# Kernel tuning notes

Hardware: AMD Instinct MI355X
Metric: run time of the kernel (lower is better)

Reference implementation:

```python
import jax, jax.numpy as jnp
import numpy as np

B, T, D_MODEL = 2, 192, 512
N_HEADS, D_HEAD = 8, 64
IGNORE = -1000000.0


def setup_inputs() -> dict:
    key = jax.random.key(0)
    ks = jax.random.split(key, 5)
    s = 0.02
    return {
        "x": jax.random.normal(ks[0], (B, T, D_MODEL), dtype=jnp.float32),
        "Wkkq": jax.random.normal(ks[1], (D_MODEL, 3 * N_HEADS * D_HEAD), dtype=jnp.float32) * s,
        "bkkq": jnp.zeros((3 * N_HEADS * D_HEAD,), jnp.float32),
        "Wv1": jax.random.normal(ks[2], (D_MODEL, N_HEADS * D_HEAD), dtype=jnp.float32) * s,
        "bv1": jnp.zeros((N_HEADS * D_HEAD,), jnp.float32),
        "Wv2": jax.random.normal(ks[3], (D_MODEL, N_HEADS * D_HEAD), dtype=jnp.float32) * s,
        "bv2": jnp.zeros((N_HEADS * D_HEAD,), jnp.float32),
        "Wout": jax.random.normal(ks[4], (N_HEADS * D_HEAD, D_MODEL), dtype=jnp.float32) * s,
        "bout": jnp.zeros((D_MODEL,), jnp.float32),
    }


def reference(x, Wkkq, bkkq, Wv1, bv1, Wv2, bv2, Wout, bout):
    b, ts, _ = x.shape
    kkq = x @ Wkkq + bkkq                          # [b, t, 3*n*h]
    k1, k2, q = jnp.split(kkq, 3, axis=-1)
    rs = lambda a: a.reshape(b, ts, N_HEADS, D_HEAD)  # b p n h
    k1, k2, q = rs(k1), rs(k2), rs(q)

    v1 = (x @ Wv1 + bv1).reshape(b, ts, N_HEADS, D_HEAD)
    v2 = (x @ Wv2 + bv2).reshape(b, ts, N_HEADS, D_HEAD)

    # third-order scores: [b, n, s, t, q]
    score_qk = jnp.einsum('btnh,bqnh->bntq', k2, q)   # [b, n, t, q]
    score_kk = jnp.einsum('bsnh,btnh->bnst', k1, k2)  # [b, n, s, t]
    score = score_qk[:, :, None, :, :] + score_kk[..., None]  # [b,n,s,t,q]

    idx = jnp.arange(ts)
    # causal mask: (t > q) | (s > q)  over axes (s, t, q)
    mask = (idx[:, None, None] > idx[None, None, :]) | (idx[None, :, None] > idx[None, None, :])
    score = jnp.where(mask[None, None], IGNORE, score)

    # b n s t q -> b n q (s t), scale by d_head, softmax over flattened (s,t)
    score = jnp.transpose(score, (0, 1, 4, 2, 3)).reshape(b, N_HEADS, ts, ts * ts)
    attn = jax.nn.softmax(score / D_HEAD, axis=-1)

    # v[b, p, t, n, h] = silu(v1)[b,p,n,h] * v2[b,t,n,h]
    v = jax.nn.silu(v1)[:, :, None] * v2[:, None]     # [b, p, t, n, h]
    v = jnp.transpose(v, (0, 3, 4, 1, 2)).reshape(b, N_HEADS, D_HEAD, ts * ts)

    z = jnp.einsum('bnql,bnhl->bqnh', attn, v)        # [b, q, n, h]
    out = z.reshape(b, ts, N_HEADS * D_HEAD) @ Wout + bout
    return out
```

## Files before the change

kernel.cpp:

```cpp
#include <hip/hip_runtime.h>
#include <hip/hip_bf16.h>


constexpr int Tn = 192;
constexpr int DM = 512;
constexpr int NH = 8;
constexpr int HD = 64;
constexpr int TT = Tn * Tn;
constexpr int NCc = 6;
constexpr int CSc = 32;

typedef __bf16 bf16_t;
typedef bf16_t bf16x8 __attribute__((ext_vector_type(8)));
typedef float  f32x4  __attribute__((ext_vector_type(4)));

struct bf16pair { bf16_t h, l; };
__device__ __forceinline__ bf16pair split_bf16(float v) {
    bf16pair r;
    r.h = (bf16_t)v;
    r.l = (bf16_t)(v - (float)r.h);
    return r;
}

__global__ __launch_bounds__(256) void k_projm(
    const float* __restrict__ x,
    const float* __restrict__ Wkkq, const float* __restrict__ Wv1,
    const float* __restrict__ Wv2,
    const float* __restrict__ bkkq, const float* __restrict__ bv1,
    const float* __restrict__ bv2,
    float* __restrict__ k1, float* __restrict__ k2, float* __restrict__ qv,
    float* __restrict__ sv1, float* __restrict__ v2o)
{
    const int bx = blockIdx.x, by = blockIdx.y;
    const int tid = threadIdx.x;
    const int w = tid >> 6, lane = tid & 63;
    const int wm = w & 1, wn = w >> 1;
    const int lr = lane & 15, lk = (lane >> 4) * 8;

    const float* Wp; int ldw, cloc;
    if (bx < 48)      { Wp = Wkkq; ldw = 1536; cloc = bx * 32; }
    else if (bx < 64) { Wp = Wv1;  ldw = 512;  cloc = bx * 32 - 1536; }
    else              { Wp = Wv2;  ldw = 512;  cloc = bx * 32 - 2048; }

    const int arow = by * 32 + wm * 16 + lr;
    const int bcol = cloc + wn * 16 + lr;
    const float* xrow = x + arow * DM;

    f32x4 acc = {0.f,0.f,0.f,0.f};
    bf16x8 A_ah, A_al, A_bh, A_bl;
    bf16x8 B_ah, B_al, B_bh, B_bl;

#define PLD(P_, KS) do { const int ko_ = (KS) * 32 + lk;                                  \
    const float4 u0 = *reinterpret_cast<const float4*>(&xrow[ko_]);                       \
    const float4 u1 = *reinterpret_cast<const float4*>(&xrow[ko_ + 4]);                   \
    const float* wp_ = Wp + ko_ * ldw + bcol;                                             \
    const float w0_ = wp_[0],       w1_ = wp_[ldw],     w2_ = wp_[2 * ldw];               \
    const float w3_ = wp_[3 * ldw], w4_ = wp_[4 * ldw], w5_ = wp_[5 * ldw];               \
    const float w6_ = wp_[6 * ldw], w7_ = wp_[7 * ldw];                                   \
    bf16pair t0_ = split_bf16(u0.x), t1_ = split_bf16(u0.y);                              \
    bf16pair t2_ = split_bf16(u0.z), t3_ = split_bf16(u0.w);                              \
    bf16pair t4_ = split_bf16(u1.x), t5_ = split_bf16(u1.y);                              \
    bf16pair t6_ = split_bf16(u1.z), t7_ = split_bf16(u1.w);                              \
    P_##ah[0] = t0_.h; P_##al[0] = t0_.l; P_##ah[1] = t1_.h; P_##al[1] = t1_.l;           \
    P_##ah[2] = t2_.h; P_##al[2] = t2_.l; P_##ah[3] = t3_.h; P_##al[3] = t3_.l;           \
    P_##ah[4] = t4_.h; P_##al[4] = t4_.l; P_##ah[5] = t5_.h; P_##al[5] = t5_.l;           \
    P_##ah[6] = t6_.h; P_##al[6] = t6_.l; P_##ah[7] = t7_.h; P_##al[7] = t7_.l;           \
    bf16pair s0_ = split_bf16(w0_), s1_ = split_bf16(w1_);                                \
    bf16pair s2_ = split_bf16(w2_), s3_ = split_bf16(w3_);                                \
    bf16pair s4_ = split_bf16(w4_), s5_ = split_bf16(w5_);                                \
    bf16pair s6_ = split_bf16(w6_), s7_ = split_bf16(w7_);                                \
    P_##bh[0] = s0_.h; P_##bl[0] = s0_.l; P_##bh[1] = s1_.h; P_##bl[1] = s1_.l;           \
    P_##bh[2] = s2_.h; P_##bl[2] = s2_.l; P_##bh[3] = s3_.h; P_##bl[3] = s3_.l;           \
    P_##bh[4] = s4_.h; P_##bl[4] = s4_.l; P_##bh[5] = s5_.h; P_##bl[5] = s5_.l;           \
    P_##bh[6] = s6_.h; P_##bl[6] = s6_.l; P_##bh[7] = s7_.h; P_##bl[7] = s7_.l; } while (0)
#define PMM(P_) do {                                                                    \
    acc = __builtin_amdgcn_mfma_f32_16x16x32_bf16(P_##ah, P_##bh, acc, 0, 0, 0);        \
    acc = __builtin_amdgcn_mfma_f32_16x16x32_bf16(P_##ah, P_##bl, acc, 0, 0, 0);        \
    acc = __builtin_amdgcn_mfma_f32_16x16x32_bf16(P_##al, P_##bh, acc, 0, 0, 0); } while (0)
#define PSTEP(P_, KN) do { PMM(P_); if ((KN) < 16) PLD(P_, KN); } while (0)

    PLD(A_, 0); PLD(B_, 1);
    PSTEP(A_, 2);  PSTEP(B_, 3);  PSTEP(A_, 4);  PSTEP(B_, 5);
    PSTEP(A_, 6);  PSTEP(B_, 7);  PSTEP(A_, 8);  PSTEP(B_, 9);
    PSTEP(A_, 10); PSTEP(B_, 11); PSTEP(A_, 12); PSTEP(B_, 13);
    PSTEP(A_, 14); PSTEP(B_, 15); PSTEP(A_, 16); PSTEP(B_, 17);
#undef PLD
#undef PMM
#undef PSTEP

    const int gcol = bx * 32 + wn * 16 + lr;
#pragma unroll
    for (int r = 0; r < 4; ++r) {
        const int row = by * 32 + wm * 16 + (lane >> 4) * 4 + r;
        const int b = row / Tn, t = row % Tn;
        const float a = acc[r];
        if (gcol < 1536) {
            const float val = a + bkkq[gcol];
            const int third = gcol >> 9, nh = gcol & 511, n = nh >> 6, hh = nh & 63;
            float* dst = (third == 0) ? k1 : (third == 1) ? k2 : qv;
            dst[((b * NH + n) * Tn + t) * HD + hh] = val;
        } else if (gcol < 2048) {
            const int c = gcol - 1536;
            float val = a + bv1[c];
            val = val / (1.f + __expf(-val));
            sv1[((b * NH + (c >> 6)) * Tn + t) * HD + (c & 63)] = val;
        } else {
            const int c = gcol - 2048;
            v2o[((b * NH + (c >> 6)) * Tn + t) * HD + (c & 63)] = a + bv2[c];
        }
    }
}

__global__ __launch_bounds__(256) void k_scoresP(
    const float* __restrict__ k1, const float* __restrict__ k2,
    const float* __restrict__ qv, const float* __restrict__ sv1,
    float* __restrict__ Ekk, float* __restrict__ Eqk,
    float* __restrict__ P, float* __restrict__ gP)
{
    const int bn = blockIdx.y;
    int bx = blockIdx.x;
    const int mat = (bx >= 36) ? 1 : 0;
    if (mat) bx -= 36;
    const int st = bx / 6, tt = bx % 6;
    const float* A  = ((mat == 0) ? k1 : qv) + bn * Tn * HD;
    const float* Bm = k2 + bn * Tn * HD;
    float* E = ((mat == 0) ? Ekk : Eqk) + bn * TT;

    __shared__ float As[32][65], Bs[32][65], Vs[32][65];
    __shared__ float Es[32][33];
    const int tid = threadIdx.x;
    for (int i = tid; i < 32 * 64; i += 256) {
        const int r = i >> 6, h = i & 63;
        As[r][h] = A[(st * 32 + r) * HD + h];
        Bs[r][h] = Bm[(tt * 32 + r) * HD + h];
        if (mat == 0) Vs[r][h] = sv1[bn * Tn * HD + (st * 32 + r) * HD + h];
    }
    __syncthreads();

    const int tx = tid & 15, ty = tid >> 4;
    const int r0 = ty * 2, c0 = tx * 2;
    float a00 = 0.f, a01 = 0.f, a10 = 0.f, a11 = 0.f;
#pragma unroll
    for (int h = 0; h < 64; ++h) {
        const float ar0 = As[r0][h], ar1 = As[r0 + 1][h];
        const float bc0 = Bs[c0][h], bc1 = Bs[c0 + 1][h];
        a00 = fmaf(ar0, bc0, a00); a01 = fmaf(ar0, bc1, a01);
        a10 = fmaf(ar1, bc0, a10); a11 = fmaf(ar1, bc1, a11);
    }
    constexpr float sc = 1.f / 64.f;
    const float e00 = __expf(a00 * sc), e01 = __expf(a01 * sc);
    const float e10 = __expf(a10 * sc), e11 = __expf(a11 * sc);
    const int gr = st * 32 + r0, gc = tt * 32 + c0;
    E[(gr)     * Tn + gc]     = e00;
    E[(gr)     * Tn + gc + 1] = e01;
    E[(gr + 1) * Tn + gc]     = e10;
    E[(gr + 1) * Tn + gc + 1] = e11;

    if (mat == 0) {
        Es[r0][c0] = e00; Es[r0][c0 + 1] = e01;
        Es[r0 + 1][c0] = e10; Es[r0 + 1][c0 + 1] = e11;
        __syncthreads();

        const int h   = tid >> 2;
        const int tp0 = (tid & 3) * 8;
        float p[8] = {0.f,0.f,0.f,0.f,0.f,0.f,0.f,0.f};
        for (int s = 0; s < 32; ++s) {
            const float a = Vs[s][h];
#pragma unroll
            for (int j = 0; j < 8; ++j) p[j] = fmaf(Es[s][tp0 + j], a, p[j]);
        }
        float* pd = P + ((bn * NCc + st) * HD + h) * Tn + tt * 32 + tp0;
        *reinterpret_cast<float4*>(&pd[0]) = make_float4(p[0], p[1], p[2], p[3]);
        *reinterpret_cast<float4*>(&pd[4]) = make_float4(p[4], p[5], p[6], p[7]);

        if (tid < 32) {
            float s = 0.f;
#pragma unroll
            for (int ss = 0; ss < 32; ++ss) s += Es[ss][tid];
            gP[(bn * NCc + st) * Tn + tt * 32 + tid] = s;
        }
    }
}

__global__ __launch_bounds__(256) void k_attn2(
    const float* __restrict__ Ekk, const float* __restrict__ Eqk,
    const float* __restrict__ sv1, const float* __restrict__ v2,
    const float* __restrict__ P,   const float* __restrict__ gP,
    float* __restrict__ z)
{
    const int hq = blockIdx.x;
    const int qt = blockIdx.y;
    const int bn = blockIdx.z;
    const int b = bn >> 3, n = bn & 7;
    const int tid = threadIdx.x;
    const int tg  = tid & 15;
    const int hh  = tid >> 4;
    const int h   = hq * 16 + hh;
    const int t0  = tg * 12;
    const int q0  = qt * 12;
    const int cb  = q0 >> 5;

    const float* ekk = Ekk + bn * TT;
    const float* eqk = Eqk + bn * TT;
    const float* s1  = sv1 + bn * Tn * HD;
    const float* vv  = v2  + bn * Tn * HD;

    float G[12], g[12];
#pragma unroll
    for (int j = 0; j < 12; ++j) { G[j] = 0.f; g[j] = 0.f; }

    for (int c = 0; c < cb; ++c) {
        const float* pb = P  + ((bn * NCc + c) * HD + h) * Tn + t0;
        const float* gb = gP + (bn * NCc + c) * Tn + t0;
#pragma unroll
        for (int jj = 0; jj < 3; ++jj) {
            const float4 pv = *reinterpret_cast<const float4*>(&pb[4 * jj]);
            G[4*jj+0] += pv.x; G[4*jj+1] += pv.y; G[4*jj+2] += pv.z; G[4*jj+3] += pv.w;
            const float4 gv = *reinterpret_cast<const float4*>(&gb[4 * jj]);
            g[4*jj+0] += gv.x; g[4*jj+1] += gv.y; g[4*jj+2] += gv.z; g[4*jj+3] += gv.w;
        }
    }

    float vvr[12];
#pragma unroll
    for (int j = 0; j < 12; ++j) vvr[j] = vv[(t0 + j) * HD + h];

    for (int s = CSc * cb; s < q0; ++s) {
        const float a = s1[s * HD + h];
        const float* ek = ekk + s * Tn + t0;
#pragma unroll
        for (int jj = 0; jj < 3; ++jj) {
            const float4 ev = *reinterpret_cast<const float4*>(&ek[4 * jj]);
            G[4*jj+0] = fmaf(ev.x, a, G[4*jj+0]); g[4*jj+0] += ev.x;
            G[4*jj+1] = fmaf(ev.y, a, G[4*jj+1]); g[4*jj+1] += ev.y;
            G[4*jj+2] = fmaf(ev.z, a, G[4*jj+2]); g[4*jj+2] += ev.z;
            G[4*jj+3] = fmaf(ev.w, a, G[4*jj+3]); g[4*jj+3] += ev.w;
        }
    }

    for (int q = q0; q < q0 + 12; ++q) {
        {
            const float a = s1[q * HD + h];
            const float* ek = ekk + q * Tn + t0;
#pragma unroll
            for (int jj = 0; jj < 3; ++jj) {
                const float4 ev = *reinterpret_cast<const float4*>(&ek[4 * jj]);
                G[4*jj+0] = fmaf(ev.x, a, G[4*jj+0]); g[4*jj+0] += ev.x;
                G[4*jj+1] = fmaf(ev.y, a, G[4*jj+1]); g[4*jj+1] += ev.y;
                G[4*jj+2] = fmaf(ev.z, a, G[4*jj+2]); g[4*jj+2] += ev.z;
                G[4*jj+3] = fmaf(ev.w, a, G[4*jj+3]); g[4*jj+3] += ev.w;
            }
        }
        const float* eq = eqk + q * Tn + t0;
        float zp = 0.f, Zp = 0.f;
#pragma unroll
        for (int jj = 0; jj < 3; ++jj) {
            const float4 ev = *reinterpret_cast<const float4*>(&eq[4 * jj]);
            const float e0 = (t0 + 4*jj + 0 <= q) ? ev.x : 0.f;
            const float e1 = (t0 + 4*jj + 1 <= q) ? ev.y : 0.f;
            const float e2 = (t0 + 4*jj + 2 <= q) ? ev.z : 0.f;
            const float e3 = (t0 + 4*jj + 3 <= q) ? ev.w : 0.f;
            zp = fmaf(e0 * vvr[4*jj+0], G[4*jj+0], zp); Zp = fmaf(e0, g[4*jj+0], Zp);
            zp = fmaf(e1 * vvr[4*jj+1], G[4*jj+1], zp); Zp = fmaf(e1, g[4*jj+1], Zp);
            zp = fmaf(e2 * vvr[4*jj+2], G[4*jj+2], zp); Zp = fmaf(e2, g[4*jj+2], Zp);
            zp = fmaf(e3 * vvr[4*jj+3], G[4*jj+3], zp); Zp = fmaf(e3, g[4*jj+3], Zp);
        }
        zp += __shfl_xor(zp, 1); zp += __shfl_xor(zp, 2);
        zp += __shfl_xor(zp, 4); zp += __shfl_xor(zp, 8);
        Zp += __shfl_xor(Zp, 1); Zp += __shfl_xor(Zp, 2);
        Zp += __shfl_xor(Zp, 4); Zp += __shfl_xor(Zp, 8);
        if (tg == 0) z[((b * Tn + q) * NH + n) * HD + h] = zp / Zp;
    }
}

__global__ __launch_bounds__(256) void k_outm(
    const float* __restrict__ z, const float* __restrict__ Wout,
    const float* __restrict__ bout, float* __restrict__ out)
{
    const int bx = blockIdx.x, by = blockIdx.y;
    const int tid = threadIdx.x;
    const int w = tid >> 6, lane = tid & 63;
    const int lr = lane & 15, lk = (lane >> 4) * 8;
    const int arow = by * 16 + lr;
    const int bcol = bx * 64 + w * 16 + lr;
    const float* zrow = z + arow * DM;

    f32x4 acc = {0.f,0.f,0.f,0.f};
    bf16x8 A_ah, A_al, A_bh, A_bl;
    bf16x8 B_ah, B_al, B_bh, B_bl;

#define OLD(P_, KS) do { const int ko_ = (KS) * 32 + lk;                                  \
    const float4 u0 = *reinterpret_cast<const float4*>(&zrow[ko_]);                       \
    const float4 u1 = *reinterpret_cast<const float4*>(&zrow[ko_ + 4]);                   \
    const float* wp_ = Wout + ko_ * DM + bcol;                                            \
    const float w0_ = wp_[0],      w1_ = wp_[DM],     w2_ = wp_[2 * DM];                  \
    const float w3_ = wp_[3 * DM], w4_ = wp_[4 * DM], w5_ = wp_[5 * DM];                  \
    const float w6_ = wp_[6 * DM], w7_ = wp_[7 * DM];                                     \
    bf16pair t0_ = split_bf16(u0.x), t1_ = split_bf16(u0.y);                              \
    bf16pair t2_ = split_bf16(u0.z), t3_ = split_bf16(u0.w);                              \
    bf16pair t4_ = split_bf16(u1.x), t5_ = split_bf16(u1.y);                              \
    bf16pair t6_ = split_bf16(u1.z), t7_ = split_bf16(u1.w);                              \
    P_##ah[0] = t0_.h; P_##al[0] = t0_.l; P_##ah[1] = t1_.h; P_##al[1] = t1_.l;           \
    P_##ah[2] = t2_.h; P_##al[2] = t2_.l; P_##ah[3] = t3_.h; P_##al[3] = t3_.l;           \
    P_##ah[4] = t4_.h; P_##al[4] = t4_.l; P_##ah[5] = t5_.h; P_##al[5] = t5_.l;           \
    P_##ah[6] = t6_.h; P_##al[6] = t6_.l; P_##ah[7] = t7_.h; P_##al[7] = t7_.l;           \
    bf16pair s0_ = split_bf16(w0_), s1_ = split_bf16(w1_);                                \
    bf16pair s2_ = split_bf16(w2_), s3_ = split_bf16(w3_);                                \
    bf16pair s4_ = split_bf16(w4_), s5_ = split_bf16(w5_);                                \
    bf16pair s6_ = split_bf16(w6_), s7_ = split_bf16(w7_);                                \
    P_##bh[0] = s0_.h; P_##bl[0] = s0_.l; P_##bh[1] = s1_.h; P_##bl[1] = s1_.l;           \
    P_##bh[2] = s2_.h; P_##bl[2] = s2_.l; P_##bh[3] = s3_.h; P_##bl[3] = s3_.l;           \
    P_##bh[4] = s4_.h; P_##bl[4] = s4_.l; P_##bh[5] = s5_.h; P_##bl[5] = s5_.l;           \
    P_##bh[6] = s6_.h; P_##bl[6] = s6_.l; P_##bh[7] = s7_.h; P_##bl[7] = s7_.l; } while (0)
#define OMM(P_) do {                                                                   \
    acc = __builtin_amdgcn_mfma_f32_16x16x32_bf16(P_##ah, P_##bh, acc, 0, 0, 0);       \
    acc = __builtin_amdgcn_mfma_f32_16x16x32_bf16(P_##ah, P_##bl, acc, 0, 0, 0);       \
    acc = __builtin_amdgcn_mfma_f32_16x16x32_bf16(P_##al, P_##bh, acc, 0, 0, 0); } while (0)
#define OSTEP(P_, KN) do { OMM(P_); if ((KN) < 16) OLD(P_, KN); } while (0)

    OLD(A_, 0); OLD(B_, 1);
    OSTEP(A_, 2);  OSTEP(B_, 3);  OSTEP(A_, 4);  OSTEP(B_, 5);
    OSTEP(A_, 6);  OSTEP(B_, 7);  OSTEP(A_, 8);  OSTEP(B_, 9);
    OSTEP(A_, 10); OSTEP(B_, 11); OSTEP(A_, 12); OSTEP(B_, 13);
    OSTEP(A_, 14); OSTEP(B_, 15); OSTEP(A_, 16); OSTEP(B_, 17);
#undef OLD
#undef OMM
#undef OSTEP

#pragma unroll
    for (int r = 0; r < 4; ++r) {
        const int row = by * 16 + (lane >> 4) * 4 + r;
        out[row * DM + bcol] = acc[r] + bout[bcol];
    }
}

extern "C" void kernel_launch(void* const* d_in, const int* in_sizes, int n_in,
                              void* d_out, int out_size, void* d_ws, size_t ws_size,
                              hipStream_t stream) {
    const float* x    = (const float*)d_in[0];
    const float* Wkkq = (const float*)d_in[1];
    const float* bkkq = (const float*)d_in[2];
    const float* Wv1  = (const float*)d_in[3];
    const float* bv1  = (const float*)d_in[4];
    const float* Wv2  = (const float*)d_in[5];
    const float* bv2  = (const float*)d_in[6];
    const float* Wout = (const float*)d_in[7];
    const float* bout = (const float*)d_in[8];
    float* out = (float*)d_out;

    float* ws  = (float*)d_ws;
    float* k1  = ws;
    float* k2  = k1  + 196608;
    float* qv  = k2  + 196608;
    float* sv1 = qv  + 196608;
    float* v2  = sv1 + 196608;
    float* z   = v2  + 196608;
    float* Ekk = z   + 196608;
    float* Eqk = Ekk + 589824;
    float* P   = Eqk + 589824;
    float* gP  = P   + 1179648;

    k_projm  <<<dim3(80, 12),    256, 0, stream>>>(x, Wkkq, Wv1, Wv2,
                                                   bkkq, bv1, bv2,
                                                   k1, k2, qv, sv1, v2);
    k_scoresP<<<dim3(72, 16),    256, 0, stream>>>(k1, k2, qv, sv1, Ekk, Eqk, P, gP);
    k_attn2  <<<dim3(4, 16, 16), 256, 0, stream>>>(Ekk, Eqk, sv1, v2, P, gP, z);
    k_outm   <<<dim3(8, 24),     256, 0, stream>>>(z, Wout, bout, out);
}
```

Measured before the change: 83.98 us.

## Fuse four kernels into one persistent cooperative kernel with grid syncs

```diff
diff --git a/kernel.cpp b/kernel.cpp
--- a/kernel.cpp
+++ b/kernel.cpp
@@ -1,5 +1,8 @@
 #include <hip/hip_runtime.h>
 #include <hip/hip_bf16.h>
+#include <hip/hip_cooperative_groups.h>
+
+namespace cg = cooperative_groups;
 
 
 constexpr int Tn = 192;
@@ -22,33 +25,35 @@
     return r;
 }
 
-__global__ __launch_bounds__(256) void k_projm(
+__device__ __forceinline__ void phase1(
     const float* __restrict__ x,
     const float* __restrict__ Wkkq, const float* __restrict__ Wv1,
     const float* __restrict__ Wv2,
     const float* __restrict__ bkkq, const float* __restrict__ bv1,
     const float* __restrict__ bv2,
     float* __restrict__ k1, float* __restrict__ k2, float* __restrict__ qv,
-    float* __restrict__ sv1, float* __restrict__ v2o)
-{
-    const int bx = blockIdx.x, by = blockIdx.y;
-    const int tid = threadIdx.x;
+    float* __restrict__ sv1, float* __restrict__ v2o,
+    int bid0, int nblk, int tid)
+{
     const int w = tid >> 6, lane = tid & 63;
     const int wm = w & 1, wn = w >> 1;
     const int lr = lane & 15, lk = (lane >> 4) * 8;
 
-    const float* Wp; int ldw, cloc;
-    if (bx < 48)      { Wp = Wkkq; ldw = 1536; cloc = bx * 32; }
-    else if (bx < 64) { Wp = Wv1;  ldw = 512;  cloc = bx * 32 - 1536; }
-    else              { Wp = Wv2;  ldw = 512;  cloc = bx * 32 - 2048; }
-
-    const int arow = by * 32 + wm * 16 + lr;
-    const int bcol = cloc + wn * 16 + lr;
-    const float* xrow = x + arow * DM;
-
-    f32x4 acc = {0.f,0.f,0.f,0.f};
-    bf16x8 A_ah, A_al, A_bh, A_bl;
-    bf16x8 B_ah, B_al, B_bh, B_bl;
+    for (int wi = bid0; wi < 960; wi += nblk) {
+        const int bx = wi % 80, by = wi / 80;
+
+        const float* Wp; int ldw, cloc;
+        if (bx < 48)      { Wp = Wkkq; ldw = 1536; cloc = bx * 32; }
+        else if (bx < 64) { Wp = Wv1;  ldw = 512;  cloc = bx * 32 - 1536; }
+        else              { Wp = Wv2;  ldw = 512;  cloc = bx * 32 - 2048; }
+
+        const int arow = by * 32 + wm * 16 + lr;
+        const int bcol = cloc + wn * 16 + lr;
+        const float* xrow = x + arow * DM;
+
+        f32x4 acc = {0.f,0.f,0.f,0.f};
+        bf16x8 A_ah, A_al, A_bh, A_bl;
+        bf16x8 B_ah, B_al, B_bh, B_bl;
 
 #define PLD(P_, KS) do { const int ko_ = (KS) * 32 + lk;                                  \
     const float4 u0 = *reinterpret_cast<const float4*>(&xrow[ko_]);                       \
@@ -79,169 +84,160 @@
     acc = __builtin_amdgcn_mfma_f32_16x16x32_bf16(P_##al, P_##bh, acc, 0, 0, 0); } while (0)
 #define PSTEP(P_, KN) do { PMM(P_); if ((KN) < 16) PLD(P_, KN); } while (0)
 
-    PLD(A_, 0); PLD(B_, 1);
-    PSTEP(A_, 2);  PSTEP(B_, 3);  PSTEP(A_, 4);  PSTEP(B_, 5);
-    PSTEP(A_, 6);  PSTEP(B_, 7);  PSTEP(A_, 8);  PSTEP(B_, 9);
-    PSTEP(A_, 10); PSTEP(B_, 11); PSTEP(A_, 12); PSTEP(B_, 13);
-    PSTEP(A_, 14); PSTEP(B_, 15); PSTEP(A_, 16); PSTEP(B_, 17);
+        PLD(A_, 0); PLD(B_, 1);
+        PSTEP(A_, 2);  PSTEP(B_, 3);  PSTEP(A_, 4);  PSTEP(B_, 5);
+        PSTEP(A_, 6);  PSTEP(B_, 7);  PSTEP(A_, 8);  PSTEP(B_, 9);
+        PSTEP(A_, 10); PSTEP(B_, 11); PSTEP(A_, 12); PSTEP(B_, 13);
+        PSTEP(A_, 14); PSTEP(B_, 15); PSTEP(A_, 16); PSTEP(B_, 17);
 #undef PLD
 #undef PMM
 #undef PSTEP
 
-    const int gcol = bx * 32 + wn * 16 + lr;
-#pragma unroll
-    for (int r = 0; r < 4; ++r) {
-        const int row = by * 32 + wm * 16 + (lane >> 4) * 4 + r;
-        const int b = row / Tn, t = row % Tn;
-        const float a = acc[r];
-        if (gcol < 1536) {
-            const float val = a + bkkq[gcol];
-            const int third = gcol >> 9, nh = gcol & 511, n = nh >> 6, hh = nh & 63;
-            float* dst = (third == 0) ? k1 : (third == 1) ? k2 : qv;
-            dst[((b * NH + n) * Tn + t) * HD + hh] = val;
-        } else if (gcol < 2048) {
-            const int c = gcol - 1536;
-            float val = a + bv1[c];
-            val = val / (1.f + __expf(-val));
-            sv1[((b * NH + (c >> 6)) * Tn + t) * HD + (c & 63)] = val;
-        } else {
-            const int c = gcol - 2048;
-            v2o[((b * NH + (c >> 6)) * Tn + t) * HD + (c & 63)] = a + bv2[c];
-        }
-    }
-}
-
-__global__ __launch_bounds__(256) void k_scoresP(
+        const int gcol = bx * 32 + wn * 16 + lr;
+#pragma unroll
+        for (int r = 0; r < 4; ++r) {
+            const int row = by * 32 + wm * 16 + (lane >> 4) * 4 + r;
+            const int b = row / Tn, t = row % Tn;
+            const float a = acc[r];
+            if (gcol < 1536) {
+                const float val = a + bkkq[gcol];
+                const int third = gcol >> 9, nh = gcol & 511, n = nh >> 6, hh = nh & 63;
+                float* dst = (third == 0) ? k1 : (third == 1) ? k2 : qv;
+                dst[((b * NH + n) * Tn + t) * HD + hh] = val;
+            } else if (gcol < 2048) {
+                const int c = gcol - 1536;
+                float val = a + bv1[c];
+                val = val / (1.f + __expf(-val));
+                sv1[((b * NH + (c >> 6)) * Tn + t) * HD + (c & 63)] = val;
+            } else {
+                const int c = gcol - 2048;
+                v2o[((b * NH + (c >> 6)) * Tn + t) * HD + (c & 63)] = a + bv2[c];
+            }
+        }
+    }
+}
+
+__device__ __forceinline__ void phase2(
     const float* __restrict__ k1, const float* __restrict__ k2,
     const float* __restrict__ qv, const float* __restrict__ sv1,
     float* __restrict__ Ekk, float* __restrict__ Eqk,
-    float* __restrict__ P, float* __restrict__ gP)
-{
-    const int bn = blockIdx.y;
-    int bx = blockIdx.x;
-    const int mat = (bx >= 36) ? 1 : 0;
-    if (mat) bx -= 36;
-    const int st = bx / 6, tt = bx % 6;
-    const float* A  = ((mat == 0) ? k1 : qv) + bn * Tn * HD;
-    const float* Bm = k2 + bn * Tn * HD;
-    float* E = ((mat == 0) ? Ekk : Eqk) + bn * TT;
-
+    float* __restrict__ P, float* __restrict__ gP,
+    int bid0, int nblk, int tid)
+{
     __shared__ float As[32][65], Bs[32][65], Vs[32][65];
     __shared__ float Es[32][33];
-    const int tid = threadIdx.x;
-    for (int i = tid; i < 32 * 64; i += 256) {
-        const int r = i >> 6, h = i & 63;
-        As[r][h] = A[(st * 32 + r) * HD + h];
-        Bs[r][h] = Bm[(tt * 32 + r) * HD + h];
-        if (mat == 0) Vs[r][h] = sv1[bn * Tn * HD + (st * 32 + r) * HD + h];
-    }
-    __syncthreads();
-
-    const int tx = tid & 15, ty = tid >> 4;
-    const int r0 = ty * 2, c0 = tx * 2;
-    float a00 = 0.f, a01 = 0.f, a10 = 0.f, a11 = 0.f;
-#pragma unroll
-    for (int h = 0; h < 64; ++h) {
-        const float ar0 = As[r0][h], ar1 = As[r0 + 1][h];
-        const float bc0 = Bs[c0][h], bc1 = Bs[c0 + 1][h];
-        a00 = fmaf(ar0, bc0, a00); a01 = fmaf(ar0, bc1, a01);
-        a10 = fmaf(ar1, bc0, a10); a11 = fmaf(ar1, bc1, a11);
-    }
-    constexpr float sc = 1.f / 64.f;
-    const float e00 = __expf(a00 * sc), e01 = __expf(a01 * sc);
-    const float e10 = __expf(a10 * sc), e11 = __expf(a11 * sc);
-    const int gr = st * 32 + r0, gc = tt * 32 + c0;
-    E[(gr)     * Tn + gc]     = e00;
-    E[(gr)     * Tn + gc + 1] = e01;
-    E[(gr + 1) * Tn + gc]     = e10;
-    E[(gr + 1) * Tn + gc + 1] = e11;
-
-    if (mat == 0) {
-        Es[r0][c0] = e00; Es[r0][c0 + 1] = e01;
-        Es[r0 + 1][c0] = e10; Es[r0 + 1][c0 + 1] = e11;
+
+    for (int wi = bid0; wi < 1152; wi += nblk) {
+        const int bn = wi / 72;
+        int bx = wi % 72;
+        const int mat = (bx >= 36) ? 1 : 0;
+        if (mat) bx -= 36;
+        const int st = bx / 6, tt = bx % 6;
+        const float* A  = ((mat == 0) ? k1 : qv) + bn * Tn * HD;
+        const float* Bm = k2 + bn * Tn * HD;
+        float* E = ((mat == 0) ? Ekk : Eqk) + bn * TT;
+
+        for (int i = tid; i < 32 * 64; i += 256) {
+            const int r = i >> 6, h = i & 63;
+            As[r][h] = A[(st * 32 + r) * HD + h];
+            Bs[r][h] = Bm[(tt * 32 + r) * HD + h];
+            if (mat == 0) Vs[r][h] = sv1[bn * Tn * HD + (st * 32 + r) * HD + h];
+        }
         __syncthreads();
 
-        const int h   = tid >> 2;
-        const int tp0 = (tid & 3) * 8;
-        float p[8] = {0.f,0.f,0.f,0.f,0.f,0.f,0.f,0.f};
-        for (int s = 0; s < 32; ++s) {
-            const float a = Vs[s][h];
-#pragma unroll
-            for (int j = 0; j < 8; ++j) p[j] = fmaf(Es[s][tp0 + j], a, p[j]);
-        }
-        float* pd = P + ((bn * NCc + st) * HD + h) * Tn + tt * 32 + tp0;
-        *reinterpret_cast<float4*>(&pd[0]) = make_float4(p[0], p[1], p[2], p[3]);
-        *reinterpret_cast<float4*>(&pd[4]) = make_float4(p[4], p[5], p[6], p[7]);
-
-        if (tid < 32) {
-            float s = 0.f;
-#pragma unroll
-            for (int ss = 0; ss < 32; ++ss) s += Es[ss][tid];
-            gP[(bn * NCc + st) * Tn + tt * 32 + tid] = s;
-        }
-    }
-}
-
-__global__ __launch_bounds__(256) void k_attn2(
+        const int tx = tid & 15, ty = tid >> 4;
+        const int r0 = ty * 2, c0 = tx * 2;
+        float a00 = 0.f, a01 = 0.f, a10 = 0.f, a11 = 0.f;
+#pragma unroll
+        for (int h = 0; h < 64; ++h) {
+            const float ar0 = As[r0][h], ar1 = As[r0 + 1][h];
+            const float bc0 = Bs[c0][h], bc1 = Bs[c0 + 1][h];
+            a00 = fmaf(ar0, bc0, a00); a01 = fmaf(ar0, bc1, a01);
+            a10 = fmaf(ar1, bc0, a10); a11 = fmaf(ar1, bc1, a11);
+        }
+        constexpr float sc = 1.f / 64.f;
+        const float e00 = __expf(a00 * sc), e01 = __expf(a01 * sc);
+        const float e10 = __expf(a10 * sc), e11 = __expf(a11 * sc);
+        const int gr = st * 32 + r0, gc = tt * 32 + c0;
+        E[(gr)     * Tn + gc]     = e00;
+        E[(gr)     * Tn + gc + 1] = e01;
+        E[(gr + 1) * Tn + gc]     = e10;
+        E[(gr + 1) * Tn + gc + 1] = e11;
+
+        if (mat == 0) {
+            Es[r0][c0] = e00; Es[r0][c0 + 1] = e01;
+            Es[r0 + 1][c0] = e10; Es[r0 + 1][c0 + 1] = e11;
+            __syncthreads();
+
+            const int h   = tid >> 2;
+            const int tp0 = (tid & 3) * 8;
+            float p[8] = {0.f,0.f,0.f,0.f,0.f,0.f,0.f,0.f};
+            for (int s = 0; s < 32; ++s) {
+                const float a = Vs[s][h];
+#pragma unroll
+                for (int j = 0; j < 8; ++j) p[j] = fmaf(Es[s][tp0 + j], a, p[j]);
+            }
+            float* pd = P + ((bn * NCc + st) * HD + h) * Tn + tt * 32 + tp0;
+            *reinterpret_cast<float4*>(&pd[0]) = make_float4(p[0], p[1], p[2], p[3]);
+            *reinterpret_cast<float4*>(&pd[4]) = make_float4(p[4], p[5], p[6], p[7]);
+
+            if (tid < 32) {
+                float s = 0.f;
+#pragma unroll
+                for (int ss = 0; ss < 32; ++ss) s += Es[ss][tid];
+                gP[(bn * NCc + st) * Tn + tt * 32 + tid] = s;
+            }
+        }
+        __syncthreads();
+    }
+}
+
+__device__ __forceinline__ void phase3(
     const float* __restrict__ Ekk, const float* __restrict__ Eqk,
-    const float* __restrict__ sv1, const float* __restrict__ v2,
+    const float* __restrict__ sv1, const float* __restrict__ v2o,
     const float* __restrict__ P,   const float* __restrict__ gP,
-    float* __restrict__ z)
-{
-    const int hq = blockIdx.x;
-    const int qt = blockIdx.y;
-    const int bn = blockIdx.z;
-    const int b = bn >> 3, n = bn & 7;
-    const int tid = threadIdx.x;
-    const int tg  = tid & 15;
-    const int hh  = tid >> 4;
-    const int h   = hq * 16 + hh;
-    const int t0  = tg * 12;
-    const int q0  = qt * 12;
-    const int cb  = q0 >> 5;
-
-    const float* ekk = Ekk + bn * TT;
-    const float* eqk = Eqk + bn * TT;
-    const float* s1  = sv1 + bn * Tn * HD;
-    const float* vv  = v2  + bn * Tn * HD;
-
-    float G[12], g[12];
-#pragma unroll
-    for (int j = 0; j < 12; ++j) { G[j] = 0.f; g[j] = 0.f; }
-
-    for (int c = 0; c < cb; ++c) {
-        const float* pb = P  + ((bn * NCc + c) * HD + h) * Tn + t0;
-        const float* gb = gP + (bn * NCc + c) * Tn + t0;
-#pragma unroll
-        for (int jj = 0; jj < 3; ++jj) {
-            const float4 pv = *reinterpret_cast<const float4*>(&pb[4 * jj]);
-            G[4*jj+0] += pv.x; G[4*jj+1] += pv.y; G[4*jj+2] += pv.z; G[4*jj+3] += pv.w;
-            const float4 gv = *reinterpret_cast<const float4*>(&gb[4 * jj]);
-            g[4*jj+0] += gv.x; g[4*jj+1] += gv.y; g[4*jj+2] += gv.z; g[4*jj+3] += gv.w;
-        }
-    }
-
-    float vvr[12];
-#pragma unroll
-    for (int j = 0; j < 12; ++j) vvr[j] = vv[(t0 + j) * HD + h];
-
-    for (int s = CSc * cb; s < q0; ++s) {
-        const float a = s1[s * HD + h];
-        const float* ek = ekk + s * Tn + t0;
-#pragma unroll
-        for (int jj = 0; jj < 3; ++jj) {
-            const float4 ev = *reinterpret_cast<const float4*>(&ek[4 * jj]);
-            G[4*jj+0] = fmaf(ev.x, a, G[4*jj+0]); g[4*jj+0] += ev.x;
-            G[4*jj+1] = fmaf(ev.y, a, G[4*jj+1]); g[4*jj+1] += ev.y;
-            G[4*jj+2] = fmaf(ev.z, a, G[4*jj+2]); g[4*jj+2] += ev.z;
-            G[4*jj+3] = fmaf(ev.w, a, G[4*jj+3]); g[4*jj+3] += ev.w;
-        }
-    }
-
-    for (int q = q0; q < q0 + 12; ++q) {
-        {
-            const float a = s1[q * HD + h];
-            const float* ek = ekk + q * Tn + t0;
+    float* __restrict__ z,
+    int bid0, int nblk, int tid)
+{
+    const int tg = tid & 15, hh = tid >> 4;
+    for (int wi = bid0; wi < 1024; wi += nblk) {
+        const int hq = wi & 3;
+        const int qt = (wi >> 2) & 15;
+        const int bn = wi >> 6;
+        const int b = bn >> 3, n = bn & 7;
+        const int h  = hq * 16 + hh;
+        const int t0 = tg * 12;
+        const int q0 = qt * 12;
+        const int cb = q0 >> 5;
+
+        const float* ekk = Ekk + bn * TT;
+        const float* eqk = Eqk + bn * TT;
+        const float* s1  = sv1 + bn * Tn * HD;
+        const float* vv  = v2o + bn * Tn * HD;
+
+        float G[12], g[12];
+#pragma unroll
+        for (int j = 0; j < 12; ++j) { G[j] = 0.f; g[j] = 0.f; }
+
+        for (int c = 0; c < cb; ++c) {
+            const float* pb = P  + ((bn * NCc + c) * HD + h) * Tn + t0;
+            const float* gb = gP + (bn * NCc + c) * Tn + t0;
+#pragma unroll
+            for (int jj = 0; jj < 3; ++jj) {
+                const float4 pv = *reinterpret_cast<const float4*>(&pb[4 * jj]);
+                G[4*jj+0] += pv.x; G[4*jj+1] += pv.y; G[4*jj+2] += pv.z; G[4*jj+3] += pv.w;
+                const float4 gv = *reinterpret_cast<const float4*>(&gb[4 * jj]);
+                g[4*jj+0] += gv.x; g[4*jj+1] += gv.y; g[4*jj+2] += gv.z; g[4*jj+3] += gv.w;
+            }
+        }
+
+        float vvr[12];
+#pragma unroll
+        for (int j = 0; j < 12; ++j) vvr[j] = vv[(t0 + j) * HD + h];
+
+        for (int s = CSc * cb; s < q0; ++s) {
+            const float a = s1[s * HD + h];
+            const float* ek = ekk + s * Tn + t0;
 #pragma unroll
             for (int jj = 0; jj < 3; ++jj) {
                 const float4 ev = *reinterpret_cast<const float4*>(&ek[4 * jj]);
@@ -251,43 +247,59 @@
                 G[4*jj+3] = fmaf(ev.w, a, G[4*jj+3]); g[4*jj+3] += ev.w;
             }
         }
-        const float* eq = eqk + q * Tn + t0;
-        float zp = 0.f, Zp = 0.f;
-#pragma unroll
-        for (int jj = 0; jj < 3; ++jj) {
-            const float4 ev = *reinterpret_cast<const float4*>(&eq[4 * jj]);
-            const float e0 = (t0 + 4*jj + 0 <= q) ? ev.x : 0.f;
-            const float e1 = (t0 + 4*jj + 1 <= q) ? ev.y : 0.f;
-            const float e2 = (t0 + 4*jj + 2 <= q) ? ev.z : 0.f;
-            const float e3 = (t0 + 4*jj + 3 <= q) ? ev.w : 0.f;
-            zp = fmaf(e0 * vvr[4*jj+0], G[4*jj+0], zp); Zp = fmaf(e0, g[4*jj+0], Zp);
-            zp = fmaf(e1 * vvr[4*jj+1], G[4*jj+1], zp); Zp = fmaf(e1, g[4*jj+1], Zp);
-            zp = fmaf(e2 * vvr[4*jj+2], G[4*jj+2], zp); Zp = fmaf(e2, g[4*jj+2], Zp);
-            zp = fmaf(e3 * vvr[4*jj+3], G[4*jj+3], zp); Zp = fmaf(e3, g[4*jj+3], Zp);
-        }
-        zp += __shfl_xor(zp, 1); zp += __shfl_xor(zp, 2);
-        zp += __shfl_xor(zp, 4); zp += __shfl_xor(zp, 8);
-        Zp += __shfl_xor(Zp, 1); Zp += __shfl_xor(Zp, 2);
-        Zp += __shfl_xor(Zp, 4); Zp += __shfl_xor(Zp, 8);
-        if (tg == 0) z[((b * Tn + q) * NH + n) * HD + h] = zp / Zp;
-    }
-}
-
-__global__ __launch_bounds__(256) void k_outm(
+
+        for (int q = q0; q < q0 + 12; ++q) {
+            {
+                const float a = s1[q * HD + h];
+                const float* ek = ekk + q * Tn + t0;
+#pragma unroll
+                for (int jj = 0; jj < 3; ++jj) {
+                    const float4 ev = *reinterpret_cast<const float4*>(&ek[4 * jj]);
+                    G[4*jj+0] = fmaf(ev.x, a, G[4*jj+0]); g[4*jj+0] += ev.x;
+                    G[4*jj+1] = fmaf(ev.y, a, G[4*jj+1]); g[4*jj+1] += ev.y;
+                    G[4*jj+2] = fmaf(ev.z, a, G[4*jj+2]); g[4*jj+2] += ev.z;
+                    G[4*jj+3] = fmaf(ev.w, a, G[4*jj+3]); g[4*jj+3] += ev.w;
+                }
+            }
+            const float* eq = eqk + q * Tn + t0;
+            float zp = 0.f, Zp = 0.f;
+#pragma unroll
+            for (int jj = 0; jj < 3; ++jj) {
+                const float4 ev = *reinterpret_cast<const float4*>(&eq[4 * jj]);
+                const float e0 = (t0 + 4*jj + 0 <= q) ? ev.x : 0.f;
+                const float e1 = (t0 + 4*jj + 1 <= q) ? ev.y : 0.f;
+                const float e2 = (t0 + 4*jj + 2 <= q) ? ev.z : 0.f;
+                const float e3 = (t0 + 4*jj + 3 <= q) ? ev.w : 0.f;
+                zp = fmaf(e0 * vvr[4*jj+0], G[4*jj+0], zp); Zp = fmaf(e0, g[4*jj+0], Zp);
+                zp = fmaf(e1 * vvr[4*jj+1], G[4*jj+1], zp); Zp = fmaf(e1, g[4*jj+1], Zp);
+                zp = fmaf(e2 * vvr[4*jj+2], G[4*jj+2], zp); Zp = fmaf(e2, g[4*jj+2], Zp);
+                zp = fmaf(e3 * vvr[4*jj+3], G[4*jj+3], zp); Zp = fmaf(e3, g[4*jj+3], Zp);
+            }
+            zp += __shfl_xor(zp, 1); zp += __shfl_xor(zp, 2);
+            zp += __shfl_xor(zp, 4); zp += __shfl_xor(zp, 8);
+            Zp += __shfl_xor(Zp, 1); Zp += __shfl_xor(Zp, 2);
+            Zp += __shfl_xor(Zp, 4); Zp += __shfl_xor(Zp, 8);
+            if (tg == 0) z[((b * Tn + q) * NH + n) * HD + h] = zp / Zp;
+        }
+    }
+}
+
+__device__ __forceinline__ void phase4(
     const float* __restrict__ z, const float* __restrict__ Wout,
-    const float* __restrict__ bout, float* __restrict__ out)
-{
-    const int bx = blockIdx.x, by = blockIdx.y;
-    const int tid = threadIdx.x;
+    const float* __restrict__ bout, float* __restrict__ out,
+    int bid0, int nblk, int tid)
+{
     const int w = tid >> 6, lane = tid & 63;
     const int lr = lane & 15, lk = (lane >> 4) * 8;
-    const int arow = by * 16 + lr;
-    const int bcol = bx * 64 + w * 16 + lr;
-    const float* zrow = z + arow * DM;
-
-    f32x4 acc = {0.f,0.f,0.f,0.f};
-    bf16x8 A_ah, A_al, A_bh, A_bl;
-    bf16x8 B_ah, B_al, B_bh, B_bl;
+    for (int wi = bid0; wi < 192; wi += nblk) {
+        const int bx = wi % 8, by = wi / 8;
+        const int arow = by * 16 + lr;
+        const int bcol = bx * 64 + w * 16 + lr;
+        const float* zrow = z + arow * DM;
+
+        f32x4 acc = {0.f,0.f,0.f,0.f};
+        bf16x8 A_ah, A_al, A_bh, A_bl;
+        bf16x8 B_ah, B_al, B_bh, B_bl;
 
 #define OLD(P_, KS) do { const int ko_ = (KS) * 32 + lk;                                  \
     const float4 u0 = *reinterpret_cast<const float4*>(&zrow[ko_]);                       \
@@ -318,20 +330,83 @@
     acc = __builtin_amdgcn_mfma_f32_16x16x32_bf16(P_##al, P_##bh, acc, 0, 0, 0); } while (0)
 #define OSTEP(P_, KN) do { OMM(P_); if ((KN) < 16) OLD(P_, KN); } while (0)
 
-    OLD(A_, 0); OLD(B_, 1);
-    OSTEP(A_, 2);  OSTEP(B_, 3);  OSTEP(A_, 4);  OSTEP(B_, 5);
-    OSTEP(A_, 6);  OSTEP(B_, 7);  OSTEP(A_, 8);  OSTEP(B_, 9);
-    OSTEP(A_, 10); OSTEP(B_, 11); OSTEP(A_, 12); OSTEP(B_, 13);
-    OSTEP(A_, 14); OSTEP(B_, 15); OSTEP(A_, 16); OSTEP(B_, 17);
+        OLD(A_, 0); OLD(B_, 1);
+        OSTEP(A_, 2);  OSTEP(B_, 3);  OSTEP(A_, 4);  OSTEP(B_, 5);
+        OSTEP(A_, 6);  OSTEP(B_, 7);  OSTEP(A_, 8);  OSTEP(B_, 9);
+        OSTEP(A_, 10); OSTEP(B_, 11); OSTEP(A_, 12); OSTEP(B_, 13);
+        OSTEP(A_, 14); OSTEP(B_, 15); OSTEP(A_, 16); OSTEP(B_, 17);
 #undef OLD
 #undef OMM
 #undef OSTEP
 
 #pragma unroll
-    for (int r = 0; r < 4; ++r) {
-        const int row = by * 16 + (lane >> 4) * 4 + r;
-        out[row * DM + bcol] = acc[r] + bout[bcol];
-    }
+        for (int r = 0; r < 4; ++r) {
+            const int row = by * 16 + (lane >> 4) * 4 + r;
+            out[row * DM + bcol] = acc[r] + bout[bcol];
+        }
+    }
+}
+
+__global__ __launch_bounds__(256, 2) void k_mega(
+    const float* __restrict__ x,
+    const float* __restrict__ Wkkq, const float* __restrict__ Wv1,
+    const float* __restrict__ Wv2,  const float* __restrict__ Wout,
+    const float* __restrict__ bkkq, const float* __restrict__ bv1,
+    const float* __restrict__ bv2,  const float* __restrict__ bout,
+    float* __restrict__ k1, float* __restrict__ k2, float* __restrict__ qv,
+    float* __restrict__ sv1, float* __restrict__ v2o, float* __restrict__ z,
+    float* __restrict__ Ekk, float* __restrict__ Eqk,
+    float* __restrict__ P,   float* __restrict__ gP,
+    float* __restrict__ out)
+{
+    cg::grid_group grid = cg::this_grid();
+    const int tid = threadIdx.x, bid = blockIdx.x, nblk = gridDim.x;
+
+    phase1(x, Wkkq, Wv1, Wv2, bkkq, bv1, bv2, k1, k2, qv, sv1, v2o, bid, nblk, tid);
+    grid.sync();
+    phase2(k1, k2, qv, sv1, Ekk, Eqk, P, gP, bid, nblk, tid);
+    grid.sync();
+    phase3(Ekk, Eqk, sv1, v2o, P, gP, z, bid, nblk, tid);
+    grid.sync();
+    phase4(z, Wout, bout, out, bid, nblk, tid);
+}
+
+__global__ __launch_bounds__(256) void k_p1(
+    const float* __restrict__ x,
+    const float* __restrict__ Wkkq, const float* __restrict__ Wv1,
+    const float* __restrict__ Wv2,
+    const float* __restrict__ bkkq, const float* __restrict__ bv1,
+    const float* __restrict__ bv2,
+    float* __restrict__ k1, float* __restrict__ k2, float* __restrict__ qv,
+    float* __restrict__ sv1, float* __restrict__ v2o)
+{
+    phase1(x, Wkkq, Wv1, Wv2, bkkq, bv1, bv2, k1, k2, qv, sv1, v2o,
+           blockIdx.x, gridDim.x, threadIdx.x);
+}
+
+__global__ __launch_bounds__(256) void k_p2(
+    const float* __restrict__ k1, const float* __restrict__ k2,
+    const float* __restrict__ qv, const float* __restrict__ sv1,
+    float* __restrict__ Ekk, float* __restrict__ Eqk,
+    float* __restrict__ P, float* __restrict__ gP)
+{
+    phase2(k1, k2, qv, sv1, Ekk, Eqk, P, gP, blockIdx.x, gridDim.x, threadIdx.x);
+}
+
+__global__ __launch_bounds__(256) void k_p3(
+    const float* __restrict__ Ekk, const float* __restrict__ Eqk,
+    const float* __restrict__ sv1, const float* __restrict__ v2o,
+    const float* __restrict__ P,   const float* __restrict__ gP,
+    float* __restrict__ z)
+{
+    phase3(Ekk, Eqk, sv1, v2o, P, gP, z, blockIdx.x, gridDim.x, threadIdx.x);
+}
+
+__global__ __launch_bounds__(256) void k_p4(
+    const float* __restrict__ z, const float* __restrict__ Wout,
+    const float* __restrict__ bout, float* __restrict__ out)
+{
+    phase4(z, Wout, bout, out, blockIdx.x, gridDim.x, threadIdx.x);
 }
 
 extern "C" void kernel_launch(void* const* d_in, const int* in_sizes, int n_in,
@@ -360,10 +435,27 @@
     float* P   = Eqk + 589824;
     float* gP  = P   + 1179648;
 
-    k_projm  <<<dim3(80, 12),    256, 0, stream>>>(x, Wkkq, Wv1, Wv2,
-                                                   bkkq, bv1, bv2,
-                                                   k1, k2, qv, sv1, v2);
-    k_scoresP<<<dim3(72, 16),    256, 0, stream>>>(k1, k2, qv, sv1, Ekk, Eqk, P, gP);
-    k_attn2  <<<dim3(4, 16, 16), 256, 0, stream>>>(Ekk, Eqk, sv1, v2, P, gP, z);
-    k_outm   <<<dim3(8, 24),     256, 0, stream>>>(z, Wout, bout, out);
-}
+    void* args[] = {
+        (void*)&x, (void*)&Wkkq, (void*)&Wv1, (void*)&Wv2, (void*)&Wout,
+        (void*)&bkkq, (void*)&bv1, (void*)&bv2, (void*)&bout,
+        (void*)&k1, (void*)&k2, (void*)&qv, (void*)&sv1, (void*)&v2,
+        (void*)&z, (void*)&Ekk, (void*)&Eqk, (void*)&P, (void*)&gP,
+        (void*)&out
+    };
+
+    hipError_t err = hipLaunchCooperativeKernel((void*)k_mega, dim3(512), dim3(256),
+                                                args, 0, stream);
+    if (err != hipSuccess) {
+        (void)hipGetLastError();
+        err = hipLaunchCooperativeKernel((void*)k_mega, dim3(256), dim3(256),
+                                         args, 0, stream);
+    }
+    if (err != hipSuccess) {
+        (void)hipGetLastError();
+        k_p1<<<dim3(960),  256, 0, stream>>>(x, Wkkq, Wv1, Wv2, bkkq, bv1, bv2,
+                                             k1, k2, qv, sv1, v2);
+        k_p2<<<dim3(1152), 256, 0, stream>>>(k1, k2, qv, sv1, Ekk, Eqk, P, gP);
+        k_p3<<<dim3(1024), 256, 0, stream>>>(Ekk, Eqk, sv1, v2, P, gP, z);
+        k_p4<<<dim3(192),  256, 0, stream>>>(z, Wout, bout, out);
+    }
+}
```

New measurement: 279.5 us. 3.33x slower.
